# Kernel optimization log

Hardware: AMD Instinct MI355X
Metric: run time of the kernel (lower is better)

## Reference

```python
import jax, jax.numpy as jnp
import numpy as np

T, B, L, F, H = 32, 32, 128, 512, 1024
SCALE = 1.0 / np.sqrt(float(L))  # 1/sqrt(max_demonstration_length)


def _lstm_step(h, c, x, W_ih, W_hh, b_ih, b_hh):
    # PyTorch LSTM gate order: i, f, g, o
    gates = x @ W_ih.T + b_ih + h @ W_hh.T + b_hh
    i, f, g, o = jnp.split(gates, 4, axis=-1)
    c = jax.nn.sigmoid(f) * c + jax.nn.sigmoid(i) * jnp.tanh(g)
    h = jax.nn.sigmoid(o) * jnp.tanh(c)
    return h, c


def setup_inputs() -> dict:
    key = jax.random.key(0)
    ks = jax.random.split(key, 20)
    s = 0.02
    d = {
        'demonstration': jax.random.normal(ks[0], (T, B, L, F), jnp.float32),
        'demonstration_lengths': jax.random.randint(ks[1], (B,), 0, L),
        'current_obs': jax.random.normal(ks[2], (T, B, F), jnp.float32),
        'h0': jnp.zeros((1, B, H), jnp.float32),
        'c0': jnp.zeros((1, B, H), jnp.float32),
        # demonstration_encoder LSTM(F -> H)
        'enc_W_ih': jax.random.normal(ks[3], (4 * H, F), jnp.float32) * s,
        'enc_W_hh': jax.random.normal(ks[4], (4 * H, H), jnp.float32) * s,
        'enc_b_ih': jnp.zeros((4 * H,), jnp.float32),
        'enc_b_hh': jnp.zeros((4 * H,), jnp.float32),
        # attn Linear(H -> H)
        'attn_W': jax.random.normal(ks[5], (H, H), jnp.float32) * s,
        'attn_b': jnp.zeros((H,), jnp.float32),
        # attn_combine MLP: (F + H) -> 4H -> H
        'mlp_W1': jax.random.normal(ks[6], (4 * H, F + H), jnp.float32) * s,
        'mlp_b1': jnp.zeros((4 * H,), jnp.float32),
        'mlp_W2': jax.random.normal(ks[7], (H, 4 * H), jnp.float32) * s,
        'mlp_b2': jnp.zeros((H,), jnp.float32),
        # recurrent LSTM(H -> H)
        'lstm_W_ih': jax.random.normal(ks[8], (4 * H, H), jnp.float32) * s,
        'lstm_W_hh': jax.random.normal(ks[9], (4 * H, H), jnp.float32) * s,
        'lstm_b_ih': jnp.zeros((4 * H,), jnp.float32),
        'lstm_b_hh': jnp.zeros((4 * H,), jnp.float32),
    }
    return d


def reference(demonstration, demonstration_lengths, current_obs, h0, c0,
              enc_W_ih, enc_W_hh, enc_b_ih, enc_b_hh,
              attn_W, attn_b, mlp_W1, mlp_b1, mlp_W2, mlp_b2,
              lstm_W_ih, lstm_W_hh, lstm_b_ih, lstm_b_hh):
    # Encode demonstration[0] (B, L, F) with an LSTM over the L axis.
    x_demo = jnp.transpose(demonstration[0], (1, 0, 2))  # (L, B, F)

    def enc(carry, xt):
        h, c = carry
        h, c = _lstm_step(h, c, xt, enc_W_ih, enc_W_hh, enc_b_ih, enc_b_hh)
        return (h, c), h

    z0 = jnp.zeros((B, H), demonstration.dtype)
    _, demo_enc = jax.lax.scan(enc, (z0, z0), x_demo)  # (L, B, H)
    demo_enc = jnp.transpose(demo_enc, (1, 0, 2))       # (B, L, H)

    # attn(demo_enc) is t-invariant; hoist it out of the loop (same math).
    attn_proj = demo_enc @ attn_W.T + attn_b            # (B, L, H)

    mask = (jnp.arange(L)[None, :] < demonstration_lengths[:, None])
    mask = mask.at[:, 0].set(True)                      # (B, L)

    def step(carry, obs_t):
        h, c = carry  # (B, H)
        scores = jnp.einsum('blh,bh->bl', attn_proj, h) * SCALE
        scores = jnp.where(mask, scores, -jnp.inf)
        w = jax.nn.softmax(scores, axis=-1)             # (B, L)
        ctx = jnp.einsum('bl,blh->bh', w, demo_enc)     # (B, H)
        z = jnp.concatenate([ctx, obs_t], axis=-1)      # (B, H+F)
        m = jax.nn.relu(z @ mlp_W1.T + mlp_b1)          # MLP hidden relu
        x = jax.nn.relu(m @ mlp_W2.T + mlp_b2)          # outer relu in forward
        h, c = _lstm_step(h, c, x, lstm_W_ih, lstm_W_hh, lstm_b_ih, lstm_b_hh)
        return (h, c), h

    (hT, cT), q = jax.lax.scan(step, (h0[0], c0[0]), current_obs)
    return q, hT[None], cT[None]
```

## Files before the change

### kernel.cpp

```cpp
#include <hip/hip_runtime.h>

typedef unsigned short u16;
typedef unsigned int   u32;
typedef short s8v __attribute__((ext_vector_type(8)));
typedef short s4v __attribute__((ext_vector_type(4)));
typedef float f4v __attribute__((ext_vector_type(4)));

#define TT 32
#define BB 32
#define LL 128
#define FF 512
#define HH 1024
#define G4 4096
#define SCALE_ 0.08838834764831845f

__device__ __forceinline__ u16 f2bf(float f){
  u32 u = __float_as_uint(f);
  u32 r = u + 0x7fffu + ((u >> 16) & 1u);
  return (u16)(r >> 16);
}
__device__ __forceinline__ float bf2f(u16 s){ return __uint_as_float(((u32)s) << 16); }
__device__ __forceinline__ float sigf(float x){ return 1.f / (1.f + __expf(-x)); }

__device__ __forceinline__ void mfma16(f4v& d, s8v a, s8v b){
  asm("v_mfma_f32_16x16x32_bf16 %0, %1, %2, %0" : "+v"(d) : "v"(a), "v"(b));
}

typedef __attribute__((address_space(3))) u32 as3u32;
typedef __attribute__((address_space(1))) u32 as1u32;
__device__ __forceinline__ void glds16(const u16* g, u16* l){
  __builtin_amdgcn_global_load_lds((const as1u32*)g, (as3u32*)l, 16, 0, 0);
}

__device__ __forceinline__ void stcc_u16(u16* p, u16 v){
  u32 vv = v;
  asm volatile("global_store_short %0, %1, off sc0 sc1" :: "v"(p), "v"(vv) : "memory");
}
__device__ __forceinline__ void stcc_u32(void* p, u32 v){
  asm volatile("global_store_dword %0, %1, off sc0 sc1" :: "v"(p), "v"(v) : "memory");
}
__device__ __forceinline__ void stcc_f32(float* p, float v){
  asm volatile("global_store_dword %0, %1, off sc0 sc1" :: "v"(p), "v"(v) : "memory");
}
__device__ __forceinline__ u32 poll_ld(const u32* p){
  u32 v;
  asm volatile("global_load_dword %0, %1, off sc0 sc1\n\ts_waitcnt vmcnt(0)"
               : "=v"(v) : "v"(p) : "memory");
  return v;
}

__device__ __forceinline__ void gbar(u32* cnt, u32 nblk, u32& epoch){
  asm volatile("s_waitcnt vmcnt(0)" ::: "memory");
  __syncthreads();
  ++epoch;
  if (threadIdx.x == 0){
    atomicAdd(cnt, 1u);
    u32 target = epoch * nblk;
    while (poll_ld(cnt) < target) __builtin_amdgcn_s_sleep(1);
  }
  __syncthreads();
}

__device__ __forceinline__ void stage512_issueS(const u16* __restrict__ src, s8v* tmp, int rstride){
  const int tid = threadIdx.x;
  const int row = tid >> 4, s0 = tid & 15;
  const u16* p = src + (size_t)row * rstride + s0 * 8;
  #pragma unroll
  for (int i = 0; i < 8; i++) tmp[i] = *(const s8v*)(p + i * 128);
}
__device__ __forceinline__ void stage512_commit(const s8v* tmp, u16* lds){
  const int tid = threadIdx.x;
  const int row = tid >> 4, s0 = tid & 15;
  char* base = (char*)lds + (row << 11);
  u32 x = (u32)(row & 15) << 4;
  #pragma unroll
  for (int i = 0; i < 8; i++){
    u32 cb = (u32)(s0 + 16 * i) << 4;
    *(s8v*)(base + (cb ^ x)) = tmp[i];
  }
}
__device__ __forceinline__ s8v ldsA(const u16* lds, int row, int cb){
  return *(const s8v*)((const char*)lds + (row << 11) + (cb ^ ((row & 15) << 4)));
}

__global__ void k_convert(const float* __restrict__ src, u16* __restrict__ dst, int n){
  int i = blockIdx.x * blockDim.x + threadIdx.x;
  int st = gridDim.x * blockDim.x;
  for (; i < n; i += st) dst[i] = f2bf(src[i]);
}
__global__ void k_split_w1(const float* __restrict__ w1, u16* __restrict__ w1c, u16* __restrict__ w1o){
  int i = blockIdx.x * blockDim.x + threadIdx.x;
  int st = gridDim.x * blockDim.x;
  const int n = G4 * (FF + HH);
  for (; i < n; i += st){
    int j = i / 1536, k = i - j * 1536;
    u16 v = f2bf(w1[i]);
    if (k < HH) w1c[j * HH + k] = v;
    else        w1o[j * FF + (k - HH)] = v;
  }
}
__global__ void k_addb(const float* __restrict__ a, const float* __restrict__ b,
                       float* __restrict__ o, int n){
  int i = blockIdx.x * blockDim.x + threadIdx.x;
  int st = gridDim.x * blockDim.x;
  for (; i < n; i += st) o[i] = a[i] + b[i];
}
__global__ void k_demo_t(const float* __restrict__ d, u16* __restrict__ o){
  const int n = LL * BB * FF;
  int i = blockIdx.x * blockDim.x + threadIdx.x;
  int st = gridDim.x * blockDim.x;
  for (; i < n; i += st){
    int f = i & 511;
    int row = i >> 9;
    int l = row >> 5, b = row & 31;
    o[i] = f2bf(d[(size_t)b * (LL * FF) + l * FF + f]);
  }
}

template<int RELU>
__global__ void __launch_bounds__(256) k_gemm_bt(const u16* __restrict__ A, const u16* __restrict__ B,
        const float* __restrict__ bias, u16* __restrict__ C, int M, int N, int K)
{
  __shared__ u16 As[128 * 64];
  __shared__ u16 Bs[128 * 64];
  const int tid = threadIdx.x;
  const int lane = tid & 63, wave = tid >> 6;
  const int m0 = blockIdx.x * 128, n0 = blockIdx.y * 128;
  const int wm = wave >> 1, wn = wave & 1;
  const int lr = lane & 15, lk = (lane >> 4) * 8;
  f4v acc[4][4];
  #pragma unroll
  for (int i = 0; i < 4; i++)
    #pragma unroll
    for (int j = 0; j < 4; j++) acc[i][j] = f4v{0.f, 0.f, 0.f, 0.f};

  for (int kt = 0; kt < K; kt += 64){
    #pragma unroll
    for (int i = 0; i < 4; i++){
      int c = tid + i * 256;
      int row = c >> 3, cc = (c & 7) * 8;
      glds16(A + (size_t)(m0 + row) * K + kt + cc, &As[c * 8]);
      glds16(B + (size_t)(n0 + row) * K + kt + cc, &Bs[c * 8]);
    }
    __syncthreads();
    #pragma unroll
    for (int ks = 0; ks < 2; ++ks){
      int ko = ks * 32 + lk;
      s8v av[4], bv[4];
      #pragma unroll
      for (int m = 0; m < 4; m++) av[m] = *(const s8v*)&As[(wm * 64 + m * 16 + lr) * 64 + ko];
      #pragma unroll
      for (int n = 0; n < 4; n++) bv[n] = *(const s8v*)&Bs[(wn * 64 + n * 16 + lr) * 64 + ko];
      #pragma unroll
      for (int m = 0; m < 4; m++)
        #pragma unroll
        for (int n = 0; n < 4; n++) mfma16(acc[m][n], av[m], bv[n]);
    }
    __syncthreads();
  }
  const int r0 = (lane >> 4) * 4;
  #pragma unroll
  for (int m = 0; m < 4; m++){
    #pragma unroll
    for (int n = 0; n < 4; n++){
      int col = n0 + wn * 64 + n * 16 + lr;
      float bc = bias[col];
      #pragma unroll
      for (int r = 0; r < 4; r++){
        int row = m0 + wm * 64 + m * 16 + r0 + r;
        float v = acc[m][n][r] + bc;
        if (RELU) v = fmaxf(v, 0.f);
        C[(size_t)row * N + col] = f2bf(v);
      }
    }
  }
}

union SMemE { u16 stage[32768]; float gx[8][32][17]; };

__global__ void __launch_bounds__(512, 1) k_encoder(const u16* __restrict__ Whh, const u16* __restrict__ Xih,
      u16* __restrict__ zslot, u16* __restrict__ denc, u32* bar)
{
  __shared__ SMemE sm;
  const int nb = blockIdx.x, tid = threadIdx.x;
  const int lane = tid & 63, w = tid >> 6;
  const int jc = nb * 16;
  const int lr = lane & 15, lk = (lane >> 4) * 8;
  const int eb = tid >> 4, ejj = tid & 15;
  const int rb = (lane >> 4) * 4;

  stcc_u16(&zslot[eb * HH + jc + ejj], 0);
  float cr = 0.f;
  u32 epoch = 0;
  gbar(bar, 64, epoch);

  const int kh = (w & 1) * 512;
  const u16* Wb = Whh + (size_t)((w >> 1) * HH + jc + lr) * HH + kh + lk;
  for (int l = 0; l < LL; ++l){
    const u16* hb = (l == 0) ? zslot : (denc + (size_t)(l - 1) * (BB * HH));
    s8v ht[8];
    stage512_issueS(hb, ht, HH);
    const u16* xr = Xih + ((size_t)(l * BB + eb)) * G4 + jc + ejj;
    float xi = bf2f(xr[0]), xf = bf2f(xr[1024]), xg = bf2f(xr[2048]), xo = bf2f(xr[3072]);
    stage512_commit(ht, sm.stage);
    __syncthreads();
    f4v a0 = {0.f,0.f,0.f,0.f}, a1 = {0.f,0.f,0.f,0.f};
    #pragma unroll 8
    for (int ks = 0; ks < 16; ++ks){
      int cb = (kh + lk + ks * 32) * 2;
      s8v va0 = ldsA(sm.stage, lr,      cb);
      s8v va1 = ldsA(sm.stage, lr + 16, cb);
      s8v vb  = *(const s8v*)(Wb + ks * 32);
      mfma16(a0, va0, vb);
      mfma16(a1, va1, vb);
    }
    __syncthreads();
    #pragma unroll
    for (int r = 0; r < 4; r++){ sm.gx[w][rb + r][lr] = a0[r]; sm.gx[w][16 + rb + r][lr] = a1[r]; }
    __syncthreads();
    {
      float gi = sm.gx[0][eb][ejj] + sm.gx[1][eb][ejj] + xi;
      float gf = sm.gx[2][eb][ejj] + sm.gx[3][eb][ejj] + xf;
      float gg = sm.gx[4][eb][ejj] + sm.gx[5][eb][ejj] + xg;
      float go = sm.gx[6][eb][ejj] + sm.gx[7][eb][ejj] + xo;
      cr = sigf(gf) * cr + sigf(gi) * tanhf(gg);
      float h = sigf(go) * tanhf(cr);
      stcc_u16(&denc[(size_t)l * (BB * HH) + eb * HH + jc + ejj], f2bf(h));
    }
    gbar(bar, 64, epoch);
  }
}

union SMemD {
  u16 stage[32768];
  float gx[8][32][17];
  struct { float swt[128]; } a;
};

__global__ void __launch_bounds__(512, 1) k_decoder(
    const u16* __restrict__ aproj, const u16* __restrict__ denc, const u16* __restrict__ obsp,
    const u16* __restrict__ W1c, const u16* __restrict__ W2w, const u16* __restrict__ WihL,
    const u16* __restrict__ WhhL, const float* __restrict__ blstm, const float* __restrict__ b2,
    const float* __restrict__ h0, const float* __restrict__ c0, const int* __restrict__ lens,
    float* __restrict__ hfR, u16* __restrict__ hbR, u16* __restrict__ ctxR,
    u16* __restrict__ mbR, u16* __restrict__ xbR, float* __restrict__ scX,
    float* __restrict__ out, u32* bar)
{
  __shared__ SMemD sm;
  const int nb = blockIdx.x, tid = threadIdx.x;
  const int lane = tid & 63, w = tid >> 6;
  const int jc = nb * 16;
  const int lr = lane & 15, lk = (lane >> 4) * 8;
  const int eb = tid >> 4, ejj = tid & 15;
  const int rb = (lane >> 4) * 4;
  const int ab = nb & 31, ah = nb >> 5;

  float cr;
  {
    float hv = h0[eb * HH + jc + ejj];
    stcc_f32(&hfR[eb * HH + jc + ejj], hv);
    stcc_u16(&hbR[eb * HH + jc + ejj], f2bf(hv));
    cr = c0[eb * HH + jc + ejj];
  }
  u32 epoch = 0;
  gbar(bar, 64, epoch);

  for (int t = 0; t < TT; ++t){
    const u16* ctxS = ctxR + (size_t)t * (BB * HH);
    const u16* mbS  = mbR  + (size_t)t * (BB * G4);
    const u16* xbS  = xbR  + (size_t)t * (BB * HH);
    const u16* hbS  = hbR  + (size_t)t * (BB * HH);
    const float* hfS= hfR  + (size_t)t * (BB * HH);
    float* scT = scX + (size_t)t * (BB * 128) + ab * 128;

    {
      const int len = lens[ab];
      float hr[16];
      const float* hp = hfS + ab * HH + lane * 16;
      #pragma unroll
      for (int i = 0; i < 16; i++) hr[i] = hp[i];
      for (int i = 0; i < 8; ++i){
        int l = ah * 64 + w * 8 + i;
        const u16* ap = aproj + ((size_t)(l * BB + ab)) * HH + lane * 16;
        s8v v0 = *(const s8v*)ap;
        s8v v1 = *(const s8v*)(ap + 8);
        float s = 0.f;
        #pragma unroll
        for (int k = 0; k < 8; k++) s += bf2f((u16)v0[k]) * hr[k];
        #pragma unroll
        for (int k = 0; k < 8; k++) s += bf2f((u16)v1[k]) * hr[8 + k];
        #pragma unroll
        for (int off = 32; off > 0; off >>= 1) s += __shfl_down(s, off);
        if (lane == 0){
          s *= SCALE_;
          if (l >= len && l != 0) s = -__builtin_inff();
          stcc_f32(&scT[l], s);
        }
      }
    }
    gbar(bar, 64, epoch);

    {
      if (w == 0){
        float x0 = scT[lane], x1 = scT[lane + 64];
        float mx = fmaxf(x0, x1);
        #pragma unroll
        for (int off = 32; off > 0; off >>= 1) mx = fmaxf(mx, __shfl_xor(mx, off));
        float e0 = __expf(x0 - mx), e1 = __expf(x1 - mx);
        float smv = e0 + e1;
        #pragma unroll
        for (int off = 32; off > 0; off >>= 1) smv += __shfl_xor(smv, off);
        float inv = 1.f / smv;
        sm.a.swt[lane] = e0 * inv;
        sm.a.swt[lane + 64] = e1 * inv;
      }
      __syncthreads();
      int col = ah * 512 + tid;
      const u16* dp = denc + (size_t)ab * HH + col;
      float acc = 0.f;
      #pragma unroll 4
      for (int l = 0; l < LL; ++l)
        acc += sm.a.swt[l] * bf2f(dp[(size_t)l * (BB * HH)]);
      stcc_u16((u16*)&ctxS[ab * HH + col], f2bf(acc));
    }
    gbar(bar, 64, epoch);

    {
      s8v ct[8];
      stage512_issueS(ctxS, ct, HH);
      stage512_commit(ct, sm.stage);
      __syncthreads();
      const int col0 = nb * 64 + (w >> 1) * 16;
      const int kh = (w & 1) * 512;
      f4v a0 = {0.f,0.f,0.f,0.f}, a1 = {0.f,0.f,0.f,0.f};
      const u16* Bp = W1c + (size_t)(col0 + lr) * HH + kh + lk;
      #pragma unroll 8
      for (int ks = 0; ks < 16; ++ks){
        int cb = (kh + lk + ks * 32) * 2;
        s8v va0 = ldsA(sm.stage, lr,      cb);
        s8v va1 = ldsA(sm.stage, lr + 16, cb);
        s8v vb  = *(const s8v*)(Bp + ks * 32);
        mfma16(a0, va0, vb);
        mfma16(a1, va1, vb);
      }
      __syncthreads();
      #pragma unroll
      for (int r = 0; r < 4; r++){ sm.gx[w][rb + r][lr] = a0[r]; sm.gx[w][16 + rb + r][lr] = a1[r]; }
      __syncthreads();
      #pragma unroll
      for (int cg = 0; cg < 4; ++cg){
        int col = nb * 64 + cg * 16 + ejj;
        float v = sm.gx[2 * cg][eb][ejj] + sm.gx[2 * cg + 1][eb][ejj]
                + bf2f(obsp[((size_t)(t * BB + eb)) * G4 + col]);
        stcc_u16((u16*)&mbS[eb * G4 + col], f2bf(fmaxf(v, 0.f)));
      }
    }
    gbar(bar, 64, epoch);

    {
      f4v a0 = {0.f,0.f,0.f,0.f}, a1 = {0.f,0.f,0.f,0.f};
      for (int q = 0; q < 4; ++q){
        s8v ct[8];
        stage512_issueS(mbS + q * 1024, ct, G4);
        stage512_commit(ct, sm.stage);
        __syncthreads();
        const u16* Bp = W2w + (size_t)(jc + lr) * G4 + q * 1024 + w * 128 + lk;
        #pragma unroll
        for (int ks = 0; ks < 4; ++ks){
          int cb = (w * 128 + lk + ks * 32) * 2;
          s8v va0 = ldsA(sm.stage, lr,      cb);
          s8v va1 = ldsA(sm.stage, lr + 16, cb);
          s8v vb  = *(const s8v*)(Bp + ks * 32);
          mfma16(a0, va0, vb);
          mfma16(a1, va1, vb);
        }
        __syncthreads();
      }
      #pragma unroll
      for (int r = 0; r < 4; r++){ sm.gx[w][rb + r][lr] = a0[r]; sm.gx[w][16 + rb + r][lr] = a1[r]; }
      __syncthreads();
      {
        float v = b2[jc + ejj];
        #pragma unroll
        for (int g = 0; g < 8; ++g) v += sm.gx[g][eb][ejj];
        stcc_u16((u16*)&xbS[eb * HH + jc + ejj], f2bf(fmaxf(v, 0.f)));
      }
    }
    gbar(bar, 64, epoch);

    {
      s8v xt[8], ht[8];
      stage512_issueS(xbS, xt, HH);
      stage512_issueS(hbS, ht, HH);
      stage512_commit(xt, sm.stage);
      __syncthreads();
      const int kh = (w & 1) * 512;
      f4v a0 = {0.f,0.f,0.f,0.f}, a1 = {0.f,0.f,0.f,0.f};
      const u16* Bx = WihL + (size_t)((w >> 1) * HH + jc + lr) * HH + kh + lk;
      #pragma unroll 8
      for (int ks = 0; ks < 16; ++ks){
        int cb = (kh + lk + ks * 32) * 2;
        s8v va0 = ldsA(sm.stage, lr,      cb);
        s8v va1 = ldsA(sm.stage, lr + 16, cb);
        s8v vb  = *(const s8v*)(Bx + ks * 32);
        mfma16(a0, va0, vb);
        mfma16(a1, va1, vb);
      }
      __syncthreads();
      stage512_commit(ht, sm.stage);
      __syncthreads();
      const u16* Bh = WhhL + (size_t)((w >> 1) * HH + jc + lr) * HH + kh + lk;
      #pragma unroll 8
      for (int ks = 0; ks < 16; ++ks){
        int cb = (kh + lk + ks * 32) * 2;
        s8v va0 = ldsA(sm.stage, lr,      cb);
        s8v va1 = ldsA(sm.stage, lr + 16, cb);
        s8v vb  = *(const s8v*)(Bh + ks * 32);
        mfma16(a0, va0, vb);
        mfma16(a1, va1, vb);
      }
      __syncthreads();
      #pragma unroll
      for (int r = 0; r < 4; r++){ sm.gx[w][rb + r][lr] = a0[r]; sm.gx[w][16 + rb + r][lr] = a1[r]; }
      __syncthreads();
      {
        int col = jc + ejj;
        float gi = sm.gx[0][eb][ejj] + sm.gx[1][eb][ejj] + blstm[col];
        float gf = sm.gx[2][eb][ejj] + sm.gx[3][eb][ejj] + blstm[1024 + col];
        float gg = sm.gx[4][eb][ejj] + sm.gx[5][eb][ejj] + blstm[2048 + col];
        float go = sm.gx[6][eb][ejj] + sm.gx[7][eb][ejj] + blstm[3072 + col];
        cr = sigf(gf) * cr + sigf(gi) * tanhf(gg);
        float h = sigf(go) * tanhf(cr);
        stcc_f32(&out[(size_t)t * (BB * HH) + eb * HH + col], h);
        stcc_f32(&hfR[(size_t)(t + 1) * (BB * HH) + eb * HH + col], h);
        stcc_u16(&hbR[(size_t)(t + 1) * (BB * HH) + eb * HH + col], f2bf(h));
        if (t == TT - 1){
          stcc_f32(&out[1048576 + eb * HH + col], h);
          stcc_f32(&out[1081344 + eb * HH + col], cr);
        }
      }
    }
    gbar(bar, 64, epoch);
  }
}

static constexpr size_t oWihE = 0;
static constexpr size_t oWhhE = oWihE + 4194304;
static constexpr size_t oAttnW= oWhhE + 8388608;
static constexpr size_t oW1C  = oAttnW+ 2097152;
static constexpr size_t oW1O  = oW1C  + 8388608;
static constexpr size_t oW2   = oW1O  + 4194304;
static constexpr size_t oWihL = oW2   + 8388608;
static constexpr size_t oWhhL = oWihL + 8388608;
static constexpr size_t oBEnc = oWhhL + 8388608;
static constexpr size_t oBL   = oBEnc + 16384;
static constexpr size_t oDemoT= oBL   + 16384;
static constexpr size_t oObsB = oDemoT+ 4194304;
static constexpr size_t oXih  = oObsB + 1048576;
static constexpr size_t oObsP = oXih  + 33554432;
static constexpr size_t oDEnc = oObsP + 8388608;
static constexpr size_t oAPrj = oDEnc + 8388608;
static constexpr size_t oZE   = oAPrj + 8388608;
static constexpr size_t oHFR  = oZE   + 65536;
static constexpr size_t oHBR  = oHFR  + 4325376;
static constexpr size_t oCtxR = oHBR  + 2162688;
static constexpr size_t oMBR  = oCtxR + 2097152;
static constexpr size_t oXBR  = oMBR  + 8388608;
static constexpr size_t oScX  = oXBR  + 2097152;
static constexpr size_t oBar  = oScX  + 524288;

extern "C" void kernel_launch(void* const* d_in, const int* in_sizes, int n_in,
                              void* d_out, int out_size, void* d_ws, size_t ws_size,
                              hipStream_t stream)
{
  const float* demo = (const float*)d_in[0];
  const int*   lens = (const int*)  d_in[1];
  const float* obs  = (const float*)d_in[2];
  const float* h0   = (const float*)d_in[3];
  const float* c0   = (const float*)d_in[4];
  const float* eWih = (const float*)d_in[5];
  const float* eWhh = (const float*)d_in[6];
  const float* eBih = (const float*)d_in[7];
  const float* eBhh = (const float*)d_in[8];
  const float* aW   = (const float*)d_in[9];
  const float* aB   = (const float*)d_in[10];
  const float* W1   = (const float*)d_in[11];
  const float* B1   = (const float*)d_in[12];
  const float* W2   = (const float*)d_in[13];
  const float* B2   = (const float*)d_in[14];
  const float* lWih = (const float*)d_in[15];
  const float* lWhh = (const float*)d_in[16];
  const float* lBih = (const float*)d_in[17];
  const float* lBhh = (const float*)d_in[18];

  char* ws = (char*)d_ws;
  u16*  WihE = (u16*)(ws + oWihE);
  u16*  WhhE = (u16*)(ws + oWhhE);
  u16*  AttnW= (u16*)(ws + oAttnW);
  u16*  W1C  = (u16*)(ws + oW1C);
  u16*  W1O  = (u16*)(ws + oW1O);
  u16*  W2w  = (u16*)(ws + oW2);
  u16*  WihL = (u16*)(ws + oWihL);
  u16*  WhhL = (u16*)(ws + oWhhL);
  float* BEnc= (float*)(ws + oBEnc);
  float* BL  = (float*)(ws + oBL);
  u16*  DemoT= (u16*)(ws + oDemoT);
  u16*  ObsB = (u16*)(ws + oObsB);
  u16*  Xih  = (u16*)(ws + oXih);
  u16*  ObsP = (u16*)(ws + oObsP);
  u16*  DEnc = (u16*)(ws + oDEnc);
  u16*  APrj = (u16*)(ws + oAPrj);
  u16*  ZE   = (u16*)(ws + oZE);
  float* HFR = (float*)(ws + oHFR);
  u16*  HBR  = (u16*)(ws + oHBR);
  u16*  CtxR = (u16*)(ws + oCtxR);
  u16*  MBR  = (u16*)(ws + oMBR);
  u16*  XBR  = (u16*)(ws + oXBR);
  float* ScX = (float*)(ws + oScX);
  u32*  Bar  = (u32*)(ws + oBar);

  k_convert<<<1024, 256, 0, stream>>>(eWih, WihE, G4 * FF);
  k_convert<<<1024, 256, 0, stream>>>(eWhh, WhhE, G4 * HH);
  k_convert<<<512,  256, 0, stream>>>(aW,   AttnW, HH * HH);
  k_split_w1<<<1024, 256, 0, stream>>>(W1, W1C, W1O);
  k_convert<<<1024, 256, 0, stream>>>(W2,   W2w,  HH * G4);
  k_convert<<<1024, 256, 0, stream>>>(lWih, WihL, G4 * HH);
  k_convert<<<1024, 256, 0, stream>>>(lWhh, WhhL, G4 * HH);
  k_addb<<<16, 256, 0, stream>>>(eBih, eBhh, BEnc, G4);
  k_addb<<<16, 256, 0, stream>>>(lBih, lBhh, BL, G4);
  k_demo_t<<<1024, 256, 0, stream>>>(demo, DemoT);
  k_convert<<<512, 256, 0, stream>>>(obs, ObsB, TT * BB * FF);
  hipMemsetAsync(Bar, 0, 256, stream);

  {
    dim3 g(LL * BB / 128, G4 / 128);
    k_gemm_bt<0><<<g, 256, 0, stream>>>(DemoT, WihE, BEnc, Xih, LL * BB, G4, FF);
  }
  {
    dim3 g(TT * BB / 128, G4 / 128);
    k_gemm_bt<0><<<g, 256, 0, stream>>>(ObsB, W1O, B1, ObsP, TT * BB, G4, FF);
  }

  k_encoder<<<64, 512, 0, stream>>>(WhhE, Xih, ZE, DEnc, Bar);

  {
    dim3 g(LL * BB / 128, HH / 128);
    k_gemm_bt<0><<<g, 256, 0, stream>>>(DEnc, AttnW, aB, APrj, LL * BB, HH, HH);
  }

  k_decoder<<<64, 512, 0, stream>>>(APrj, DEnc, ObsP, W1C, W2w, WihL, WhhL,
                                    BL, B2, h0, c0, lens,
                                    HFR, HBR, CtxR, MBR, XBR, ScX,
                                    (float*)d_out, Bar + 16);
}
```

Before: 2.700 ms.

## Double threads per block in persistent encoder/decoder, splitting K across 16 waves

Raises the persistent recurrent encoder and decoder kernels from 512 to 1024 threads per block. The K reduction is split four ways instead of two across 16 waves, staging and reduction buffers are resized, and the elementwise gate math stays on the first 512 threads. The intent is to shorten each serial step's MFMA and load latency chain by adding wave-level parallelism, which matters because only 64 blocks run. In exchange the register budget per thread is tighter, more partial sums must be reduced through LDS, and half the threads sit idle during the elementwise phases.

Measured after the change: 2.676 ms. Within noise of the previous version (-0.9%).

```diff
diff --git a/kernel.cpp b/kernel.cpp
--- a/kernel.cpp
+++ b/kernel.cpp
@@ -3,7 +3,6 @@
 typedef unsigned short u16;
 typedef unsigned int   u32;
 typedef short s8v __attribute__((ext_vector_type(8)));
-typedef short s4v __attribute__((ext_vector_type(4)));
 typedef float f4v __attribute__((ext_vector_type(4)));
 
 #define TT 32
@@ -35,9 +34,6 @@
 __device__ __forceinline__ void stcc_u16(u16* p, u16 v){
   u32 vv = v;
   asm volatile("global_store_short %0, %1, off sc0 sc1" :: "v"(p), "v"(vv) : "memory");
-}
-__device__ __forceinline__ void stcc_u32(void* p, u32 v){
-  asm volatile("global_store_dword %0, %1, off sc0 sc1" :: "v"(p), "v"(v) : "memory");
 }
 __device__ __forceinline__ void stcc_f32(float* p, float v){
   asm volatile("global_store_dword %0, %1, off sc0 sc1" :: "v"(p), "v"(v) : "memory");
@@ -61,21 +57,21 @@
   __syncthreads();
 }
 
-__device__ __forceinline__ void stage512_issueS(const u16* __restrict__ src, s8v* tmp, int rstride){
+__device__ __forceinline__ void stg_issue(const u16* __restrict__ src, s8v* tmp, int rstride){
   const int tid = threadIdx.x;
-  const int row = tid >> 4, s0 = tid & 15;
+  const int row = tid >> 5, s0 = tid & 31;
   const u16* p = src + (size_t)row * rstride + s0 * 8;
   #pragma unroll
-  for (int i = 0; i < 8; i++) tmp[i] = *(const s8v*)(p + i * 128);
-}
-__device__ __forceinline__ void stage512_commit(const s8v* tmp, u16* lds){
+  for (int i = 0; i < 4; i++) tmp[i] = *(const s8v*)(p + i * 256);
+}
+__device__ __forceinline__ void stg_commit(const s8v* tmp, u16* lds){
   const int tid = threadIdx.x;
-  const int row = tid >> 4, s0 = tid & 15;
+  const int row = tid >> 5, s0 = tid & 31;
   char* base = (char*)lds + (row << 11);
   u32 x = (u32)(row & 15) << 4;
   #pragma unroll
-  for (int i = 0; i < 8; i++){
-    u32 cb = (u32)(s0 + 16 * i) << 4;
+  for (int i = 0; i < 4; i++){
+    u32 cb = (u32)(s0 + 32 * i) << 4;
     *(s8v*)(base + (cb ^ x)) = tmp[i];
   }
 }
@@ -176,9 +172,9 @@
   }
 }
 
-union SMemE { u16 stage[32768]; float gx[8][32][17]; };
-
-__global__ void __launch_bounds__(512, 1) k_encoder(const u16* __restrict__ Whh, const u16* __restrict__ Xih,
+union SMemE { u16 stage[32768]; float gx[16][32][17]; };
+
+__global__ void __launch_bounds__(1024, 4) k_encoder(const u16* __restrict__ Whh, const u16* __restrict__ Xih,
       u16* __restrict__ zslot, u16* __restrict__ denc, u32* bar)
 {
   __shared__ SMemE sm;
@@ -189,24 +185,27 @@
   const int eb = tid >> 4, ejj = tid & 15;
   const int rb = (lane >> 4) * 4;
 
-  stcc_u16(&zslot[eb * HH + jc + ejj], 0);
+  if (tid < 512) stcc_u16(&zslot[eb * HH + jc + ejj], 0);
   float cr = 0.f;
   u32 epoch = 0;
   gbar(bar, 64, epoch);
 
-  const int kh = (w & 1) * 512;
-  const u16* Wb = Whh + (size_t)((w >> 1) * HH + jc + lr) * HH + kh + lk;
+  const int kh = (w & 3) * 256;
+  const u16* Wb = Whh + (size_t)((w >> 2) * HH + jc + lr) * HH + kh + lk;
   for (int l = 0; l < LL; ++l){
     const u16* hb = (l == 0) ? zslot : (denc + (size_t)(l - 1) * (BB * HH));
-    s8v ht[8];
-    stage512_issueS(hb, ht, HH);
-    const u16* xr = Xih + ((size_t)(l * BB + eb)) * G4 + jc + ejj;
-    float xi = bf2f(xr[0]), xf = bf2f(xr[1024]), xg = bf2f(xr[2048]), xo = bf2f(xr[3072]);
-    stage512_commit(ht, sm.stage);
+    s8v ht[4];
+    stg_issue(hb, ht, HH);
+    float xi = 0, xf = 0, xg = 0, xo = 0;
+    if (tid < 512){
+      const u16* xr = Xih + ((size_t)(l * BB + eb)) * G4 + jc + ejj;
+      xi = bf2f(xr[0]); xf = bf2f(xr[1024]); xg = bf2f(xr[2048]); xo = bf2f(xr[3072]);
+    }
+    stg_commit(ht, sm.stage);
     __syncthreads();
     f4v a0 = {0.f,0.f,0.f,0.f}, a1 = {0.f,0.f,0.f,0.f};
-    #pragma unroll 8
-    for (int ks = 0; ks < 16; ++ks){
+    #pragma unroll
+    for (int ks = 0; ks < 8; ++ks){
       int cb = (kh + lk + ks * 32) * 2;
       s8v va0 = ldsA(sm.stage, lr,      cb);
       s8v va1 = ldsA(sm.stage, lr + 16, cb);
@@ -218,11 +217,11 @@
     #pragma unroll
     for (int r = 0; r < 4; r++){ sm.gx[w][rb + r][lr] = a0[r]; sm.gx[w][16 + rb + r][lr] = a1[r]; }
     __syncthreads();
-    {
-      float gi = sm.gx[0][eb][ejj] + sm.gx[1][eb][ejj] + xi;
-      float gf = sm.gx[2][eb][ejj] + sm.gx[3][eb][ejj] + xf;
-      float gg = sm.gx[4][eb][ejj] + sm.gx[5][eb][ejj] + xg;
-      float go = sm.gx[6][eb][ejj] + sm.gx[7][eb][ejj] + xo;
+    if (tid < 512){
+      float gi = sm.gx[0][eb][ejj] + sm.gx[1][eb][ejj] + sm.gx[2][eb][ejj] + sm.gx[3][eb][ejj] + xi;
+      float gf = sm.gx[4][eb][ejj] + sm.gx[5][eb][ejj] + sm.gx[6][eb][ejj] + sm.gx[7][eb][ejj] + xf;
+      float gg = sm.gx[8][eb][ejj] + sm.gx[9][eb][ejj] + sm.gx[10][eb][ejj] + sm.gx[11][eb][ejj] + xg;
+      float go = sm.gx[12][eb][ejj] + sm.gx[13][eb][ejj] + sm.gx[14][eb][ejj] + sm.gx[15][eb][ejj] + xo;
       cr = sigf(gf) * cr + sigf(gi) * tanhf(gg);
       float h = sigf(go) * tanhf(cr);
       stcc_u16(&denc[(size_t)l * (BB * HH) + eb * HH + jc + ejj], f2bf(h));
@@ -233,11 +232,11 @@
 
 union SMemD {
   u16 stage[32768];
-  float gx[8][32][17];
+  float gx[16][32][17];
   struct { float swt[128]; } a;
 };
 
-__global__ void __launch_bounds__(512, 1) k_decoder(
+__global__ void __launch_bounds__(1024, 4) k_decoder(
     const u16* __restrict__ aproj, const u16* __restrict__ denc, const u16* __restrict__ obsp,
     const u16* __restrict__ W1c, const u16* __restrict__ W2w, const u16* __restrict__ WihL,
     const u16* __restrict__ WhhL, const float* __restrict__ blstm, const float* __restrict__ b2,
@@ -255,8 +254,8 @@
   const int rb = (lane >> 4) * 4;
   const int ab = nb & 31, ah = nb >> 5;
 
-  float cr;
-  {
+  float cr = 0.f;
+  if (tid < 512){
     float hv = h0[eb * HH + jc + ejj];
     stcc_f32(&hfR[eb * HH + jc + ejj], hv);
     stcc_u16(&hbR[eb * HH + jc + ejj], f2bf(hv));
@@ -279,8 +278,9 @@
       const float* hp = hfS + ab * HH + lane * 16;
       #pragma unroll
       for (int i = 0; i < 16; i++) hr[i] = hp[i];
-      for (int i = 0; i < 8; ++i){
-        int l = ah * 64 + w * 8 + i;
+      #pragma unroll
+      for (int i = 0; i < 4; ++i){
+        int l = ah * 64 + w * 4 + i;
         const u16* ap = aproj + ((size_t)(l * BB + ab)) * HH + lane * 16;
         s8v v0 = *(const s8v*)ap;
         s8v v1 = *(const s8v*)(ap + 8);
@@ -315,27 +315,29 @@
         sm.a.swt[lane + 64] = e1 * inv;
       }
       __syncthreads();
-      int col = ah * 512 + tid;
-      const u16* dp = denc + (size_t)ab * HH + col;
-      float acc = 0.f;
-      #pragma unroll 4
-      for (int l = 0; l < LL; ++l)
-        acc += sm.a.swt[l] * bf2f(dp[(size_t)l * (BB * HH)]);
-      stcc_u16((u16*)&ctxS[ab * HH + col], f2bf(acc));
+      if (tid < 512){
+        int col = ah * 512 + tid;
+        const u16* dp = denc + (size_t)ab * HH + col;
+        float acc = 0.f;
+        #pragma unroll 4
+        for (int l = 0; l < LL; ++l)
+          acc += sm.a.swt[l] * bf2f(dp[(size_t)l * (BB * HH)]);
+        stcc_u16((u16*)&ctxS[ab * HH + col], f2bf(acc));
+      }
     }
     gbar(bar, 64, epoch);
 
     {
-      s8v ct[8];
-      stage512_issueS(ctxS, ct, HH);
-      stage512_commit(ct, sm.stage);
-      __syncthreads();
-      const int col0 = nb * 64 + (w >> 1) * 16;
-      const int kh = (w & 1) * 512;
+      s8v ct[4];
+      stg_issue(ctxS, ct, HH);
+      stg_commit(ct, sm.stage);
+      __syncthreads();
+      const int col0 = nb * 64 + (w >> 2) * 16;
+      const int kh = (w & 3) * 256;
       f4v a0 = {0.f,0.f,0.f,0.f}, a1 = {0.f,0.f,0.f,0.f};
       const u16* Bp = W1c + (size_t)(col0 + lr) * HH + kh + lk;
-      #pragma unroll 8
-      for (int ks = 0; ks < 16; ++ks){
+      #pragma unroll
+      for (int ks = 0; ks < 8; ++ks){
         int cb = (kh + lk + ks * 32) * 2;
         s8v va0 = ldsA(sm.stage, lr,      cb);
         s8v va1 = ldsA(sm.stage, lr + 16, cb);
@@ -347,12 +349,15 @@
       #pragma unroll
       for (int r = 0; r < 4; r++){ sm.gx[w][rb + r][lr] = a0[r]; sm.gx[w][16 + rb + r][lr] = a1[r]; }
       __syncthreads();
-      #pragma unroll
-      for (int cg = 0; cg < 4; ++cg){
-        int col = nb * 64 + cg * 16 + ejj;
-        float v = sm.gx[2 * cg][eb][ejj] + sm.gx[2 * cg + 1][eb][ejj]
-                + bf2f(obsp[((size_t)(t * BB + eb)) * G4 + col]);
-        stcc_u16((u16*)&mbS[eb * G4 + col], f2bf(fmaxf(v, 0.f)));
+      if (tid < 512){
+        #pragma unroll
+        for (int cg = 0; cg < 4; ++cg){
+          int col = nb * 64 + cg * 16 + ejj;
+          float v = sm.gx[4 * cg][eb][ejj] + sm.gx[4 * cg + 1][eb][ejj]
+                  + sm.gx[4 * cg + 2][eb][ejj] + sm.gx[4 * cg + 3][eb][ejj]
+                  + bf2f(obsp[((size_t)(t * BB + eb)) * G4 + col]);
+          stcc_u16((u16*)&mbS[eb * G4 + col], f2bf(fmaxf(v, 0.f)));
+        }
       }
     }
     gbar(bar, 64, epoch);
@@ -360,14 +365,14 @@
     {
       f4v a0 = {0.f,0.f,0.f,0.f}, a1 = {0.f,0.f,0.f,0.f};
       for (int q = 0; q < 4; ++q){
-        s8v ct[8];
-        stage512_issueS(mbS + q * 1024, ct, G4);
-        stage512_commit(ct, sm.stage);
+        s8v ct[4];
+        stg_issue(mbS + q * 1024, ct, G4);
+        stg_commit(ct, sm.stage);
         __syncthreads();
-        const u16* Bp = W2w + (size_t)(jc + lr) * G4 + q * 1024 + w * 128 + lk;
-        #pragma unroll
-        for (int ks = 0; ks < 4; ++ks){
-          int cb = (w * 128 + lk + ks * 32) * 2;
+        const u16* Bp = W2w + (size_t)(jc + lr) * G4 + q * 1024 + w * 64 + lk;
+        #pragma unroll
+        for (int ks = 0; ks < 2; ++ks){
+          int cb = (w * 64 + lk + ks * 32) * 2;
           s8v va0 = ldsA(sm.stage, lr,      cb);
           s8v va1 = ldsA(sm.stage, lr + 16, cb);
           s8v vb  = *(const s8v*)(Bp + ks * 32);
@@ -379,26 +384,26 @@
       #pragma unroll
       for (int r = 0; r < 4; r++){ sm.gx[w][rb + r][lr] = a0[r]; sm.gx[w][16 + rb + r][lr] = a1[r]; }
       __syncthreads();
-      {
+      if (tid < 512){
         float v = b2[jc + ejj];
         #pragma unroll
-        for (int g = 0; g < 8; ++g) v += sm.gx[g][eb][ejj];
+        for (int g = 0; g < 16; ++g) v += sm.gx[g][eb][ejj];
         stcc_u16((u16*)&xbS[eb * HH + jc + ejj], f2bf(fmaxf(v, 0.f)));
       }
     }
     gbar(bar, 64, epoch);
 
     {
-      s8v xt[8], ht[8];
-      stage512_issueS(xbS, xt, HH);
-      stage512_issueS(hbS, ht, HH);
-      stage512_commit(xt, sm.stage);
-      __syncthreads();
-      const int kh = (w & 1) * 512;
+      s8v xt[4], ht[4];
+      stg_issue(xbS, xt, HH);
+      stg_issue(hbS, ht, HH);
+      stg_commit(xt, sm.stage);
+      __syncthreads();
+      const int kh = (w & 3) * 256;
       f4v a0 = {0.f,0.f,0.f,0.f}, a1 = {0.f,0.f,0.f,0.f};
-      const u16* Bx = WihL + (size_t)((w >> 1) * HH + jc + lr) * HH + kh + lk;
-      #pragma unroll 8
-      for (int ks = 0; ks < 16; ++ks){
+      const u16* Bx = WihL + (size_t)((w >> 2) * HH + jc + lr) * HH + kh + lk;
+      #pragma unroll
+      for (int ks = 0; ks < 8; ++ks){
         int cb = (kh + lk + ks * 32) * 2;
         s8v va0 = ldsA(sm.stage, lr,      cb);
         s8v va1 = ldsA(sm.stage, lr + 16, cb);
@@ -407,11 +412,11 @@
         mfma16(a1, va1, vb);
       }
       __syncthreads();
-      stage512_commit(ht, sm.stage);
-      __syncthreads();
-      const u16* Bh = WhhL + (size_t)((w >> 1) * HH + jc + lr) * HH + kh + lk;
-      #pragma unroll 8
-      for (int ks = 0; ks < 16; ++ks){
+      stg_commit(ht, sm.stage);
+      __syncthreads();
+      const u16* Bh = WhhL + (size_t)((w >> 2) * HH + jc + lr) * HH + kh + lk;
+      #pragma unroll
+      for (int ks = 0; ks < 8; ++ks){
         int cb = (kh + lk + ks * 32) * 2;
         s8v va0 = ldsA(sm.stage, lr,      cb);
         s8v va1 = ldsA(sm.stage, lr + 16, cb);
@@ -423,12 +428,12 @@
       #pragma unroll
       for (int r = 0; r < 4; r++){ sm.gx[w][rb + r][lr] = a0[r]; sm.gx[w][16 + rb + r][lr] = a1[r]; }
       __syncthreads();
-      {
+      if (tid < 512){
         int col = jc + ejj;
-        float gi = sm.gx[0][eb][ejj] + sm.gx[1][eb][ejj] + blstm[col];
-        float gf = sm.gx[2][eb][ejj] + sm.gx[3][eb][ejj] + blstm[1024 + col];
-        float gg = sm.gx[4][eb][ejj] + sm.gx[5][eb][ejj] + blstm[2048 + col];
-        float go = sm.gx[6][eb][ejj] + sm.gx[7][eb][ejj] + blstm[3072 + col];
+        float gi = sm.gx[0][eb][ejj] + sm.gx[1][eb][ejj] + sm.gx[2][eb][ejj] + sm.gx[3][eb][ejj] + blstm[col];
+        float gf = sm.gx[4][eb][ejj] + sm.gx[5][eb][ejj] + sm.gx[6][eb][ejj] + sm.gx[7][eb][ejj] + blstm[1024 + col];
+        float gg = sm.gx[8][eb][ejj] + sm.gx[9][eb][ejj] + sm.gx[10][eb][ejj] + sm.gx[11][eb][ejj] + blstm[2048 + col];
+        float go = sm.gx[12][eb][ejj] + sm.gx[13][eb][ejj] + sm.gx[14][eb][ejj] + sm.gx[15][eb][ejj] + blstm[3072 + col];
         cr = sigf(gf) * cr + sigf(gi) * tanhf(gg);
         float h = sigf(go) * tanhf(cr);
         stcc_f32(&out[(size_t)t * (BB * HH) + eb * HH + col], h);
@@ -541,15 +546,15 @@
     k_gemm_bt<0><<<g, 256, 0, stream>>>(ObsB, W1O, B1, ObsP, TT * BB, G4, FF);
   }
 
-  k_encoder<<<64, 512, 0, stream>>>(WhhE, Xih, ZE, DEnc, Bar);
+  k_encoder<<<64, 1024, 0, stream>>>(WhhE, Xih, ZE, DEnc, Bar);
 
   {
     dim3 g(LL * BB / 128, HH / 128);
     k_gemm_bt<0><<<g, 256, 0, stream>>>(DEnc, AttnW, aB, APrj, LL * BB, HH, HH);
   }
 
-  k_decoder<<<64, 512, 0, stream>>>(APrj, DEnc, ObsP, W1C, W2w, WihL, WhhL,
-                                    BL, B2, h0, c0, lens,
-                                    HFR, HBR, CtxR, MBR, XBR, ScX,
-                                    (float*)d_out, Bar + 16);
-}
+  k_decoder<<<64, 1024, 0, stream>>>(APrj, DEnc, ObsP, W1C, W2w, WihL, WhhL,
+                                     BL, B2, h0, c0, lens,
+                                     HFR, HBR, CtxR, MBR, XBR, ScX,
+                                     (float*)d_out, Bar + 16);
+}
```
